# Optimization experiments

Measured on AMD Instinct MI355X. Metric: run time of the kernel, lower is better.

The kernel has to match this reference:

```python
import jax, jax.numpy as jnp
import numpy as np

N_HEADS = 12
HIDDEN = 768
HEAD_DIM = HIDDEN // N_HEADS
B, S = 4, 2048


def setup_inputs() -> dict:
    key = jax.random.key(0)
    ks = jax.random.split(key, 7)
    bound = 1.0 / np.sqrt(HIDDEN)  # torch nn.Linear default init range
    inputs = jax.random.normal(ks[0], (B, S, HIDDEN), dtype=jnp.float32)
    Wq = jax.random.uniform(ks[1], (HIDDEN, HIDDEN), jnp.float32, -bound, bound)
    bq = jax.random.uniform(ks[2], (HIDDEN,), jnp.float32, -bound, bound)
    Wk = jax.random.uniform(ks[3], (HIDDEN, HIDDEN), jnp.float32, -bound, bound)
    bk = jax.random.uniform(ks[4], (HIDDEN,), jnp.float32, -bound, bound)
    Wv = jax.random.uniform(ks[5], (HIDDEN, HIDDEN), jnp.float32, -bound, bound)
    bv = jax.random.uniform(ks[6], (HIDDEN,), jnp.float32, -bound, bound)
    return {"inputs": inputs, "Wq": Wq, "bq": bq, "Wk": Wk, "bk": bk, "Wv": Wv, "bv": bv}


def reference(inputs, Wq, bq, Wk, bk, Wv, bv):
    b, s, d = inputs.shape
    h, hd = N_HEADS, HEAD_DIM
    # torch Linear: x @ W^T + b; reshape to (b, s, h, hd) -> (b, h, s, hd)
    def proj(W, bias):
        y = inputs @ W.T + bias
        return y.reshape(b, s, h, hd).transpose(0, 2, 1, 3)
    q = proj(Wq, bq)
    k = proj(Wk, bk)
    v = proj(Wv, bv)
    scale = 1.0 / jnp.sqrt(jnp.asarray(hd, inputs.dtype))
    scores = jnp.einsum('bhqd,bhkd->bhqk', q, k) * scale  # [b,h,s,s] materialized as in source
    attn = jax.nn.softmax(scores, axis=-1)
    out = jnp.einsum('bhqk,bhkd->bhqd', attn, v)
    # (b, h, s, hd) -> (b, s, h*hd)
    return out.transpose(0, 2, 1, 3).reshape(b, s, d)
```

## Files before the change

kernel.cpp:

```cpp
#include <hip/hip_runtime.h>
#include <hip/hip_bf16.h>
#include <math.h>

#define NH   12
#define HD   64
#define HID  768
#define NB   4
#define SS   2048
#define MR   (NB*SS)

#define NXE  (MR*HID)
#define NWE  (HID*HID)

typedef unsigned short u16;
typedef u16   u16x8  __attribute__((ext_vector_type(8)));
typedef __bf16 bf16x8 __attribute__((ext_vector_type(8)));
typedef float f32x4  __attribute__((ext_vector_type(4)));

union V8 { uint4 v; u16 s[8]; unsigned w[4]; };

__device__ __forceinline__ float hi2f(unsigned u) {
    union { unsigned i; float f; } c; c.i = u & 0xffff0000u; return c.f;
}
__device__ __forceinline__ float lo2f(unsigned u) {
    union { unsigned i; float f; } c; c.i = u << 16; return c.f;
}
__device__ __forceinline__ u16 f2b(float f) {
    union { float f; unsigned i; } c; c.f = f;
    unsigned x = c.i + 0x7fffu + ((c.i >> 16) & 1u);
    return (u16)(x >> 16);
}
__device__ __forceinline__ unsigned pk2(float lo, float hi) {
    float2 f; f.x = lo; f.y = hi;
    union { __hip_bfloat162 h; unsigned u; } c;
    c.h = __float22bfloat162_rn(f);
    return c.u;
}
__device__ __forceinline__ f32x4 mfma16(u16x8 a, u16x8 b, f32x4 c) {
    return __builtin_amdgcn_mfma_f32_16x16x32_bf16(
        __builtin_bit_cast(bf16x8, a), __builtin_bit_cast(bf16x8, b), c, 0, 0, 0);
}
__device__ __forceinline__ void g2l16(const u16* g, u16* l) {
    __builtin_amdgcn_global_load_lds(
        (const __attribute__((address_space(1))) void*)g,
        (__attribute__((address_space(3))) void*)l, 16, 0, 0);
}

__global__ __launch_bounds__(256) void to_bf16(
    const float* __restrict__ x,  const float* __restrict__ Wq,
    const float* __restrict__ Wk, const float* __restrict__ Wv,
    u16* __restrict__ dst)
{
    const int NX4 = NXE / 4, NW4 = NWE / 4, NT4 = NX4 + 3 * NW4;
    for (int i = blockIdx.x * 256 + threadIdx.x; i < NT4; i += gridDim.x * 256) {
        const float* src; u16* d;
        if (i < NX4) { src = x + (size_t)i * 4; d = dst + (size_t)i * 4; }
        else {
            int j = i - NX4; int w = j / NW4; int r = j - w * NW4;
            const float* Ws = (w == 0) ? Wq : ((w == 1) ? Wk : Wv);
            src = Ws + (size_t)r * 4; d = dst + NXE + (size_t)w * NWE + (size_t)r * 4;
        }
        float4 f = *(const float4*)src;
        uint2 o; o.x = pk2(f.x, f.y); o.y = pk2(f.z, f.w);
        *(uint2*)d = o;
    }
}

__global__ __launch_bounds__(256, 3) void qkv_proj(
    const u16* __restrict__ xb, const u16* __restrict__ Wb,
    const float* __restrict__ bq, const float* __restrict__ bk,
    const float* __restrict__ bv, u16* __restrict__ qkv)
{
    const int wsel = blockIdx.z;
    const u16* W = Wb + (size_t)wsel * NWE;
    const float* bias = (wsel == 0) ? bq : ((wsel == 1) ? bk : bv);
    u16* out = qkv + (size_t)wsel * MR * HID;

    const int m0 = blockIdx.x * 128, n0 = blockIdx.y * 128;
    __shared__ __align__(16) u16 As[128][32];
    __shared__ __align__(16) u16 Bs[128][32];

    const int tid  = threadIdx.x;
    const int lane = tid & 63, wid = tid >> 6;
    const int quad = lane >> 4, l16 = lane & 15;
    const int wm = wid >> 1, wn = wid & 1;

    const int rA = 2 * wid * 16 + (lane >> 2);
    const int colh = (lane & 3) * 8;
    const u16* gx0 = xb + (size_t)(m0 + rA) * HID + colh;
    const u16* gx1 = gx0 + (size_t)16 * HID;
    const u16* gw0 = W  + (size_t)(n0 + rA) * HID + colh;
    const u16* gw1 = gw0 + (size_t)16 * HID;
    u16* lA0 = &As[0][0] + (2 * wid) * 512 + lane * 8;
    u16* lA1 = lA0 + 512;
    u16* lB0 = &Bs[0][0] + (2 * wid) * 512 + lane * 8;
    u16* lB1 = lB0 + 512;

    f32x4 acc[4][4] = {};

    for (int k0 = 0; k0 < HID; k0 += 32) {
        g2l16(gx0 + k0, lA0); g2l16(gx1 + k0, lA1);
        g2l16(gw0 + k0, lB0); g2l16(gw1 + k0, lB1);
        __syncthreads();
        u16x8 af[4], bf[4];
        #pragma unroll
        for (int i = 0; i < 4; i++) af[i] = *(const u16x8*)&As[wm * 64 + i * 16 + l16][quad * 8];
        #pragma unroll
        for (int j = 0; j < 4; j++) bf[j] = *(const u16x8*)&Bs[wn * 64 + j * 16 + l16][quad * 8];
        #pragma unroll
        for (int i = 0; i < 4; i++)
            #pragma unroll
            for (int j = 0; j < 4; j++)
                acc[i][j] = mfma16(af[i], bf[j], acc[i][j]);
        __syncthreads();
    }

    #pragma unroll
    for (int j = 0; j < 4; j++) {
        const int col = n0 + wn * 64 + j * 16 + l16;
        const float bb = bias[col];
        #pragma unroll
        for (int i = 0; i < 4; i++)
            #pragma unroll
            for (int r = 0; r < 4; r++) {
                const int row = m0 + wm * 64 + i * 16 + quad * 4 + r;
                out[(size_t)row * HID + col] = f2b(acc[i][j][r] + bb);
            }
    }
}

__global__ __launch_bounds__(256, 3) void attn(
    const u16* __restrict__ qkv, float* __restrict__ out)
{
    const int q0 = blockIdx.x * 128;
    const int h  = blockIdx.y;
    const int b  = blockIdx.z;

    const u16* qb = qkv + (size_t)b * SS * HID + h * HD;
    const u16* kb = qkv + (size_t)MR * HID     + (size_t)b * SS * HID + h * HD;
    const u16* vb = qkv + (size_t)2 * MR * HID + (size_t)b * SS * HID + h * HD;
    float*     ob = out + (size_t)b * SS * HID + h * HD;

    __shared__ __align__(16) u16 Ks[64][72];
    __shared__ __align__(16) u16 Vt[64][72];

    const int tid  = threadIdx.x;
    const int lane = tid & 63, wid = tid >> 6;
    const int quad = lane >> 4, l16 = lane & 15;
    const int srow = tid >> 3, scg = tid & 7;

    int prow[2];
    #pragma unroll
    for (int r2 = 0; r2 < 2; r2++) {
        const int k = r2 * 32 + srow;
        prow[r2] = ((k >> 5) << 5) | (((k >> 2) & 1) << 4) | (((k >> 3) & 3) << 2) | (k & 3);
    }

    const float QS = 0.18033688f;
    u16x8 qf[2][2];
    #pragma unroll
    for (int t = 0; t < 2; t++) {
        const int row = q0 + t * 64 + wid * 16 + l16;
        #pragma unroll
        for (int hh = 0; hh < 2; hh++) {
            V8 raw; raw.v = *(const uint4*)(qb + (size_t)row * HID + hh * 32 + quad * 8);
            uint4 p; unsigned* pp = (unsigned*)&p;
            #pragma unroll
            for (int e = 0; e < 4; e++)
                pp[e] = pk2(lo2f(raw.w[e]) * QS, hi2f(raw.w[e]) * QS);
            qf[t][hh] = __builtin_bit_cast(u16x8, p);
        }
    }

    f32x4 o2[2][4] = {};
    float lsum[2] = {0.f, 0.f};

    for (int kt = 0; kt < SS / 64; kt++) {
        #pragma unroll
        for (int r2 = 0; r2 < 2; r2++) {
            const int key = r2 * 32 + srow;
            *(uint4*)&Ks[prow[r2]][scg * 8] =
                *(const uint4*)(kb + (size_t)(kt * 64 + key) * HID + scg * 8);
            V8 t; t.v = *(const uint4*)(vb + (size_t)(kt * 64 + key) * HID + scg * 8);
            const int colp = key ^ (scg * 8);
            #pragma unroll
            for (int e = 0; e < 8; e++) Vt[scg * 8 + e][colp] = t.s[e];
        }
        __syncthreads();

        u16x8 kf[4][2];
        #pragma unroll
        for (int n = 0; n < 4; n++)
            #pragma unroll
            for (int hh = 0; hh < 2; hh++)
                kf[n][hh] = *(const u16x8*)&Ks[n * 16 + l16][hh * 32 + quad * 8];

        unsigned pkd[2][4][2];
        #pragma unroll
        for (int t = 0; t < 2; t++)
            #pragma unroll
            for (int n = 0; n < 4; n++) {
                f32x4 s = {};
                s = mfma16(kf[n][0], qf[t][0], s);
                s = mfma16(kf[n][1], qf[t][1], s);
                const float p0 = __builtin_amdgcn_exp2f(s[0] - 6.0f);
                const float p1 = __builtin_amdgcn_exp2f(s[1] - 6.0f);
                const float p2 = __builtin_amdgcn_exp2f(s[2] - 6.0f);
                const float p3 = __builtin_amdgcn_exp2f(s[3] - 6.0f);
                const unsigned w01 = pk2(p0, p1);
                const unsigned w23 = pk2(p2, p3);
                pkd[t][n][0] = w01; pkd[t][n][1] = w23;
                lsum[t] += (lo2f(w01) + hi2f(w01)) + (lo2f(w23) + hi2f(w23));
            }

        u16x8 vf[4][2];
        #pragma unroll
        for (int n2 = 0; n2 < 4; n2++) {
            const int d = n2 * 16 + l16, sz = d >> 3;
            #pragma unroll
            for (int hh = 0; hh < 2; hh++)
                vf[n2][hh] = *(const u16x8*)&Vt[d][(((hh * 4 + quad) ^ sz) & 7) * 8];
        }

        #pragma unroll
        for (int t = 0; t < 2; t++) {
            union { u16x8 v; unsigned d[4]; } bf0, bf1;
            bf0.d[0] = pkd[t][0][0]; bf0.d[1] = pkd[t][0][1];
            bf0.d[2] = pkd[t][1][0]; bf0.d[3] = pkd[t][1][1];
            bf1.d[0] = pkd[t][2][0]; bf1.d[1] = pkd[t][2][1];
            bf1.d[2] = pkd[t][3][0]; bf1.d[3] = pkd[t][3][1];
            #pragma unroll
            for (int n2 = 0; n2 < 4; n2++) {
                o2[t][n2] = mfma16(vf[n2][0], bf0.v, o2[t][n2]);
                o2[t][n2] = mfma16(vf[n2][1], bf1.v, o2[t][n2]);
            }
        }
        __syncthreads();
    }

    #pragma unroll
    for (int t = 0; t < 2; t++) {
        float rs = lsum[t];
        rs += __shfl_xor(rs, 16);
        rs += __shfl_xor(rs, 32);
        const float inv = 1.f / rs;
        const int q = q0 + t * 64 + wid * 16 + l16;
        #pragma unroll
        for (int n2 = 0; n2 < 4; n2++) {
            f32x4 w = o2[t][n2];
            w[0] *= inv; w[1] *= inv; w[2] *= inv; w[3] *= inv;
            *(f32x4*)(ob + (size_t)q * HID + n2 * 16 + quad * 4) = w;
        }
    }
}

extern "C" void kernel_launch(void* const* d_in, const int* in_sizes, int n_in,
                              void* d_out, int out_size, void* d_ws, size_t ws_size,
                              hipStream_t stream) {
    const float* x  = (const float*)d_in[0];
    const float* Wq = (const float*)d_in[1];
    const float* bq = (const float*)d_in[2];
    const float* Wk = (const float*)d_in[3];
    const float* bk = (const float*)d_in[4];
    const float* Wv = (const float*)d_in[5];
    const float* bv = (const float*)d_in[6];
    float* out = (float*)d_out;
    u16* qkv = (u16*)d_ws;
    u16* cvt = (u16*)d_out;

    to_bf16<<<1024, 256, 0, stream>>>(x, Wq, Wk, Wv, cvt);

    dim3 gp(MR / 128, HID / 128, 3);
    qkv_proj<<<gp, 256, 0, stream>>>(cvt, cvt + NXE, bq, bk, bv, qkv);

    dim3 ga(SS / 128, NH, NB);
    attn<<<ga, 256, 0, stream>>>(qkv, out);
}
```

Baseline: 204.9 us.

## Move Q scaling, K permutation and V transpose into projection epilogue

The projection GEMM epilogue now pre-scales Q by the softmax scale, writes K rows in the permuted key order the attention kernel expects, and writes V transposed per head as [b,h,d,s]. The attention kernel can then load Q directly and copy K and V tiles into shared memory with plain 16-byte stores, removing the per-element transpose scatter and the per-block Q rescaling. The cost is that the V epilogue now writes 8-byte chunks strided by the sequence length, and that Q is rounded to bf16 after scaling rather than before.

```diff
diff --git a/kernel.cpp b/kernel.cpp
--- a/kernel.cpp
+++ b/kernel.cpp
@@ -17,8 +17,6 @@
 typedef __bf16 bf16x8 __attribute__((ext_vector_type(8)));
 typedef float f32x4  __attribute__((ext_vector_type(4)));
 
-union V8 { uint4 v; u16 s[8]; unsigned w[4]; };
-
 __device__ __forceinline__ float hi2f(unsigned u) {
     union { unsigned i; float f; } c; c.i = u & 0xffff0000u; return c.f;
 }
@@ -44,6 +42,9 @@
     __builtin_amdgcn_global_load_lds(
         (const __attribute__((address_space(1))) void*)g,
         (__attribute__((address_space(3))) void*)l, 16, 0, 0);
+}
+__device__ __forceinline__ int kperm(int k) {
+    return ((k >> 5) << 5) | (((k >> 2) & 1) << 4) | (((k >> 3) & 3) << 2) | (k & 3);
 }
 
 __global__ __launch_bounds__(256) void to_bf16(
@@ -115,17 +116,38 @@
         __syncthreads();
     }
 
-    #pragma unroll
-    for (int j = 0; j < 4; j++) {
-        const int col = n0 + wn * 64 + j * 16 + l16;
-        const float bb = bias[col];
-        #pragma unroll
-        for (int i = 0; i < 4; i++)
-            #pragma unroll
-            for (int r = 0; r < 4; r++) {
-                const int row = m0 + wm * 64 + i * 16 + quad * 4 + r;
-                out[(size_t)row * HID + col] = f2b(acc[i][j][r] + bb);
+    if (wsel == 2) {
+        const int bidx = m0 >> 11;
+        const int s0 = (m0 & 2047) + wm * 64;
+        #pragma unroll
+        for (int j = 0; j < 4; j++) {
+            const int col = n0 + wn * 64 + j * 16 + l16;
+            const float bb = bias[col];
+            const int hh = col >> 6, d = col & 63;
+            u16* vrow = out + ((size_t)(bidx * NH + hh) * HD + d) * SS;
+            #pragma unroll
+            for (int i = 0; i < 4; i++) {
+                uint2 pk;
+                pk.x = pk2(acc[i][j][0] + bb, acc[i][j][1] + bb);
+                pk.y = pk2(acc[i][j][2] + bb, acc[i][j][3] + bb);
+                *(uint2*)(vrow + s0 + i * 16 + quad * 4) = pk;
             }
+        }
+    } else {
+        const float scale = (wsel == 0) ? 0.18033688f : 1.0f;
+        #pragma unroll
+        for (int j = 0; j < 4; j++) {
+            const int col = n0 + wn * 64 + j * 16 + l16;
+            const float bb = bias[col];
+            #pragma unroll
+            for (int i = 0; i < 4; i++)
+                #pragma unroll
+                for (int r = 0; r < 4; r++) {
+                    int row = m0 + wm * 64 + i * 16 + quad * 4 + r;
+                    if (wsel == 1) row = (row & ~63) | kperm(row & 63);
+                    out[(size_t)row * HID + col] = f2b((acc[i][j][r] + bb) * scale);
+                }
+        }
     }
 }
 
@@ -136,10 +158,10 @@
     const int h  = blockIdx.y;
     const int b  = blockIdx.z;
 
-    const u16* qb = qkv + (size_t)b * SS * HID + h * HD;
-    const u16* kb = qkv + (size_t)MR * HID     + (size_t)b * SS * HID + h * HD;
-    const u16* vb = qkv + (size_t)2 * MR * HID + (size_t)b * SS * HID + h * HD;
-    float*     ob = out + (size_t)b * SS * HID + h * HD;
+    const u16* qb  = qkv + (size_t)b * SS * HID + h * HD;
+    const u16* kb  = qkv + (size_t)MR * HID + (size_t)b * SS * HID + h * HD;
+    const u16* vtb = qkv + (size_t)2 * MR * HID + ((size_t)(b * NH + h) * HD) * SS;
+    float*     ob  = out + (size_t)b * SS * HID + h * HD;
 
     __shared__ __align__(16) u16 Ks[64][72];
     __shared__ __align__(16) u16 Vt[64][72];
@@ -149,27 +171,13 @@
     const int quad = lane >> 4, l16 = lane & 15;
     const int srow = tid >> 3, scg = tid & 7;
 
-    int prow[2];
-    #pragma unroll
-    for (int r2 = 0; r2 < 2; r2++) {
-        const int k = r2 * 32 + srow;
-        prow[r2] = ((k >> 5) << 5) | (((k >> 2) & 1) << 4) | (((k >> 3) & 3) << 2) | (k & 3);
-    }
-
-    const float QS = 0.18033688f;
     u16x8 qf[2][2];
     #pragma unroll
     for (int t = 0; t < 2; t++) {
         const int row = q0 + t * 64 + wid * 16 + l16;
         #pragma unroll
-        for (int hh = 0; hh < 2; hh++) {
-            V8 raw; raw.v = *(const uint4*)(qb + (size_t)row * HID + hh * 32 + quad * 8);
-            uint4 p; unsigned* pp = (unsigned*)&p;
-            #pragma unroll
-            for (int e = 0; e < 4; e++)
-                pp[e] = pk2(lo2f(raw.w[e]) * QS, hi2f(raw.w[e]) * QS);
-            qf[t][hh] = __builtin_bit_cast(u16x8, p);
-        }
+        for (int hh = 0; hh < 2; hh++)
+            qf[t][hh] = *(const u16x8*)(qb + (size_t)row * HID + hh * 32 + quad * 8);
     }
 
     f32x4 o2[2][4] = {};
@@ -178,13 +186,11 @@
     for (int kt = 0; kt < SS / 64; kt++) {
         #pragma unroll
         for (int r2 = 0; r2 < 2; r2++) {
-            const int key = r2 * 32 + srow;
-            *(uint4*)&Ks[prow[r2]][scg * 8] =
-                *(const uint4*)(kb + (size_t)(kt * 64 + key) * HID + scg * 8);
-            V8 t; t.v = *(const uint4*)(vb + (size_t)(kt * 64 + key) * HID + scg * 8);
-            const int colp = key ^ (scg * 8);
-            #pragma unroll
-            for (int e = 0; e < 8; e++) Vt[scg * 8 + e][colp] = t.s[e];
+            const int rr = r2 * 32 + srow;
+            *(uint4*)&Ks[rr][scg * 8] =
+                *(const uint4*)(kb + (size_t)(kt * 64 + rr) * HID + scg * 8);
+            *(uint4*)&Vt[rr][scg * 8] =
+                *(const uint4*)(vtb + (size_t)rr * SS + kt * 64 + scg * 8);
         }
         __syncthreads();
 
@@ -215,12 +221,10 @@
 
         u16x8 vf[4][2];
         #pragma unroll
-        for (int n2 = 0; n2 < 4; n2++) {
-            const int d = n2 * 16 + l16, sz = d >> 3;
+        for (int n2 = 0; n2 < 4; n2++)
             #pragma unroll
             for (int hh = 0; hh < 2; hh++)
-                vf[n2][hh] = *(const u16x8*)&Vt[d][(((hh * 4 + quad) ^ sz) & 7) * 8];
-        }
+                vf[n2][hh] = *(const u16x8*)&Vt[n2 * 16 + l16][hh * 32 + quad * 8];
 
         #pragma unroll
         for (int t = 0; t < 2; t++) {
```

Result: no change. 206.5 us (+0.8%).
